# Performance work log

Measured on AMD Instinct MI355X. Metric: run time of the kernel, lower is better.

Reference implementation:

```python
import jax, jax.numpy as jnp
import numpy as np

B, N, C = 8, 2048, 512

def setup_inputs() -> dict:
    key = jax.random.key(0)
    k1, k2, k3 = jax.random.split(key, 3)
    x = jax.random.normal(k1, (B, N, C), dtype=jnp.float32)
    # xavier_uniform with gain=1.414 ~ uniform(-b, b), b = gain*sqrt(6/(fan_in+fan_out))
    bw = 1.414 * np.sqrt(6.0 / (C + C))
    w = jax.random.uniform(k2, (C, C), dtype=jnp.float32, minval=-bw, maxval=bw)
    ba = 1.414 * np.sqrt(6.0 / (2 * C + 1))
    a = jax.random.uniform(k3, (2 * C, 1), dtype=jnp.float32, minval=-ba, maxval=ba)
    return {"x": x, "w": w, "a": a}

def reference(x, w, a):
    # x: [B,N,C], w: [C,C], a: [2C,1]
    C_ = w.shape[0]
    h = jnp.matmul(x, w)                      # [B,N,C]
    a1 = a[:C_, 0]                            # [C]
    a2 = a[C_:, 0]                            # [C]
    # The torch repeat/cat/view builds e_ij = LeakyReLU(a1.h_i + a2.h_j);
    # compute the same math via broadcasting (no [B,N,N,2C] tensor).
    s1 = jnp.einsum('bnc,c->bn', h, a1)       # [B,N]
    s2 = jnp.einsum('bnc,c->bn', h, a2)       # [B,N]
    e = jax.nn.leaky_relu(s1[:, :, None] + s2[:, None, :], negative_slope=0.2)  # [B,N,N]
    attention = jax.nn.softmax(e, axis=2)     # softmax over source nodes j
    # dropout is identity in eval mode (training=False)
    h_prime = jnp.matmul(attention, x)        # [B,N,C]
    return h_prime
```

## Files before the change

kernel.cpp:

```cpp
#include <hip/hip_runtime.h>
#include <math.h>

#define B_ 8
#define N_ 2048
#define C_ 512
#define G_ 64
#define L_ 32

static const size_t OFF_V1   = 0;
static const size_t OFF_V2   = OFF_V1 + 512;
static const size_t OFF_S1   = OFF_V2 + 512;
static const size_t OFF_S2   = OFF_S1 + 16384;
static const size_t OFF_Z    = OFF_S2 + 16384;
static const size_t OFF_IDX  = OFF_Z + 16384;
static const size_t OFF_P    = OFF_IDX + 16384;
static const size_t OFF_Q    = OFF_P + 16384;
static const size_t OFF_CHP  = OFF_Q + 16384;
static const size_t OFF_CHQ  = OFF_CHP + 262144;
static const size_t OFF_TOTQ = OFF_CHQ + 262144;
static const size_t OFF_EMR  = OFF_TOTQ + 4096;
static const size_t OFF_EMP  = OFF_EMR + 16384;
static const size_t OFF_EMQ  = OFF_EMP + 16384;
static const size_t OFF_POS  = OFF_EMQ + 16384;

__device__ inline float4 f4z() { return make_float4(0.f, 0.f, 0.f, 0.f); }
__device__ inline float4 fma4(float s, float4 a, float4 c) {
    c.x = fmaf(s, a.x, c.x); c.y = fmaf(s, a.y, c.y);
    c.z = fmaf(s, a.z, c.z); c.w = fmaf(s, a.w, c.w); return c;
}
__device__ inline float4 add4(float4 a, float4 b) {
    return make_float4(a.x + b.x, a.y + b.y, a.z + b.z, a.w + b.w);
}
__device__ inline float4 comb4(float fp, float4 P, float fq, float4 T, float4 Q) {
    return make_float4(fp * P.x + fq * (T.x - Q.x),
                       fp * P.y + fq * (T.y - Q.y),
                       fp * P.z + fq * (T.z - Q.z),
                       fp * P.w + fq * (T.w - Q.w));
}

__global__ __launch_bounds__(64) void k_wa(const float* __restrict__ w,
                                           const float* __restrict__ a,
                                           float* __restrict__ v1, float* __restrict__ v2) {
    int k = blockIdx.x, lane = threadIdx.x;
    float acc1 = 0.f, acc2 = 0.f;
    for (int c = lane; c < C_; c += 64) {
        float wv = w[k * C_ + c];
        acc1 += wv * a[c];
        acc2 += wv * a[C_ + c];
    }
    for (int o = 32; o > 0; o >>= 1) { acc1 += __shfl_down(acc1, o); acc2 += __shfl_down(acc2, o); }
    if (lane == 0) { v1[k] = acc1; v2[k] = acc2; }
}

__global__ __launch_bounds__(256) void k_s(const float* __restrict__ x,
                                           const float* __restrict__ v1,
                                           const float* __restrict__ v2,
                                           float* __restrict__ s1, float* __restrict__ s2) {
    __shared__ __align__(16) float sv1[C_];
    __shared__ __align__(16) float sv2[C_];
    int tid = threadIdx.x;
    for (int c = tid; c < C_; c += 256) { sv1[c] = v1[c]; sv2[c] = v2[c]; }
    __syncthreads();
    int wave = tid >> 6, lane = tid & 63;
    int r = blockIdx.x * 4 + wave;
    const float4* xr  = reinterpret_cast<const float4*>(x + (size_t)r * C_);
    const float4* w1p = reinterpret_cast<const float4*>(sv1);
    const float4* w2p = reinterpret_cast<const float4*>(sv2);
    float a1 = 0.f, a2 = 0.f;
    #pragma unroll
    for (int half = 0; half < 2; ++half) {
        int c4 = lane + half * 64;
        float4 xv = xr[c4], w1 = w1p[c4], w2 = w2p[c4];
        a1 += xv.x*w1.x + xv.y*w1.y + xv.z*w1.z + xv.w*w1.w;
        a2 += xv.x*w2.x + xv.y*w2.y + xv.z*w2.z + xv.w*w2.w;
    }
    for (int o = 32; o > 0; o >>= 1) { a1 += __shfl_down(a1, o); a2 += __shfl_down(a2, o); }
    if (lane == 0) { s1[r] = a1; s2[r] = a2; }
}

__global__ __launch_bounds__(256) void k_rank(const float* __restrict__ s2,
                                              float* __restrict__ z, int* __restrict__ idxArr,
                                              float* __restrict__ pArr, float* __restrict__ qArr) {
    __shared__ float sval[N_];
    __shared__ float sred[256];
    __shared__ int   srnk[256];
    int blk = blockIdx.x;
    int b = blk >> 5, grp = blk & 31;
    int tid = threadIdx.x;
    int le = tid & 63, qtr = tid >> 6;
    for (int i = tid; i < N_; i += 256) sval[i] = s2[(size_t)b * N_ + i];
    __syncthreads();
    int e = grp * 64 + le;
    float val = sval[e];
    int base = qtr * 512;
    int rank = 0;
    float mx = -3.4e38f;
    #pragma unroll 8
    for (int i = 0; i < 512; ++i) {
        int t = base + i;
        float v = sval[t];
        mx = fmaxf(mx, v);
        rank += (v < val) || (v == val && t < e);
    }
    srnk[tid] = rank;
    sred[tid] = mx;
    __syncthreads();
    for (int o = 128; o > 0; o >>= 1) {
        if (tid < o) sred[tid] = fmaxf(sred[tid], sred[tid + o]);
        __syncthreads();
    }
    float m2 = sred[0];
    if (qtr == 0) {
        int rk = srnk[le] + srnk[le + 64] + srnk[le + 128] + srnk[le + 192];
        float d = val - m2;
        size_t pos = (size_t)b * N_ + rk;
        z[pos]      = val;
        idxArr[pos] = e;
        pArr[pos]   = __expf(d);
        qArr[pos]   = __expf(0.2f * d);
    }
}

__global__ __launch_bounds__(512) void k_chunk(const float* __restrict__ x,
                                               const int* __restrict__ idxArr,
                                               const float* __restrict__ pArr,
                                               const float* __restrict__ qArr,
                                               float* __restrict__ chP, float* __restrict__ chQ) {
    int bg = blockIdx.x, b = bg >> 6, g = bg & 63;
    int tid = threadIdx.x;
    __shared__ int   srow[L_];
    __shared__ float spv[L_], sqv[L_];
    __shared__ float4 partP[4][128], partQ[4][128];
    if (tid < L_) {
        int j = g * L_ + tid;
        srow[tid] = idxArr[b * N_ + j];
        spv[tid]  = pArr[b * N_ + j];
        sqv[tid]  = qArr[b * N_ + j];
    }
    __syncthreads();
    int rg = tid >> 7, q = tid & 127;
    const float4* xb4 = reinterpret_cast<const float4*>(x + (size_t)b * N_ * C_);
    float4 aP = f4z(), aQ = f4z();
    #pragma unroll
    for (int i = 0; i < 8; ++i) {
        int j = rg * 8 + i;
        float4 xv = xb4[(size_t)srow[j] * 128 + q];
        aP = fma4(spv[j], xv, aP);
        aQ = fma4(sqv[j], xv, aQ);
    }
    partP[rg][q] = aP;
    partQ[rg][q] = aQ;
    __syncthreads();
    if (tid < 128) {
        float4 s = add4(add4(partP[0][tid], partP[1][tid]), add4(partP[2][tid], partP[3][tid]));
        reinterpret_cast<float4*>(chP + (size_t)bg * C_)[tid] = s;
    } else if (tid < 256) {
        int qq = tid - 128;
        float4 s = add4(add4(partQ[0][qq], partQ[1][qq]), add4(partQ[2][qq], partQ[3][qq]));
        reinterpret_cast<float4*>(chQ + (size_t)bg * C_)[qq] = s;
    }
}

__global__ __launch_bounds__(128) void k_choff(float* __restrict__ chP, float* __restrict__ chQ,
                                               float* __restrict__ totQ) {
    int t = blockIdx.x * 128 + threadIdx.x;
    int isQ = t >> 12, rem = t & 4095;
    int b = rem >> 9, c = rem & 511;
    float* arr = isQ ? chQ : chP;
    float v[G_];
    #pragma unroll
    for (int g = 0; g < G_; ++g)
        v[g] = arr[((size_t)(b * G_ + g)) * C_ + c];
    float run = 0.f;
    #pragma unroll
    for (int g = G_ - 1; g >= 0; --g) {
        float tv = v[g];
        arr[((size_t)(b * G_ + g)) * C_ + c] = run;
        run += tv;
    }
    if (isQ) totQ[b * C_ + c] = run;
}

__global__ __launch_bounds__(1024) void k_prep(const float* __restrict__ s1,
                                               const float* __restrict__ z,
                                               const float* __restrict__ pArr,
                                               const float* __restrict__ qArr,
                                               int* __restrict__ emRow,
                                               float* __restrict__ emFP,
                                               float* __restrict__ emFQ,
                                               int* __restrict__ posStart) {
    __shared__ float Ppre[2049], Qpre[2049];
    __shared__ float zv[N_];
    __shared__ int   cnt[2049];
    __shared__ int   ps[2050];
    __shared__ float wsP[16], wsQ[16], woP[16], woQ[16];
    __shared__ int   wsC[16], woC[16];
    int b = blockIdx.x, tid = threadIdx.x, lane = tid & 63, wid = tid >> 6;
    size_t ib = (size_t)b * N_;

    for (int i = tid; i < 2049; i += 1024) cnt[i] = 0;
    zv[2*tid]   = z[ib + 2*tid];
    zv[2*tid+1] = z[ib + 2*tid+1];

    float p0 = pArr[ib + 2*tid], p1 = pArr[ib + 2*tid+1];
    float q0 = qArr[ib + 2*tid], q1 = qArr[ib + 2*tid+1];
    float pv = p0 + p1, qv = q0 + q1;
    float pi = pv, qi = qv;
    for (int o = 1; o < 64; o <<= 1) {
        float tp = __shfl_up(pi, o), tq2 = __shfl_up(qi, o);
        if (lane >= o) { pi += tp; qi += tq2; }
    }
    if (lane == 63) { wsP[wid] = pi; wsQ[wid] = qi; }
    __syncthreads();
    if (wid == 0 && lane < 16) {
        float sp = wsP[lane], sq = wsQ[lane];
        float ip = sp, iq = sq;
        for (int o = 1; o < 16; o <<= 1) {
            float tp = __shfl_up(ip, o), tq2 = __shfl_up(iq, o);
            if (lane >= o) { ip += tp; iq += tq2; }
        }
        woP[lane] = ip - sp; woQ[lane] = iq - sq;
    }
    __syncthreads();
    float inclP = pi + woP[wid], inclQ = qi + woQ[wid];
    float exclP = inclP - pv,    exclQ = inclQ - qv;
    Ppre[2*tid]   = exclP;  Ppre[2*tid+1] = exclP + p0;
    Qpre[2*tid]   = exclQ;  Qpre[2*tid+1] = exclQ + q0;
    if (tid == 1023) { Ppre[2048] = inclP; Qpre[2048] = inclQ; }
    __syncthreads();

    float m2   = zv[N_ - 1];
    float Ptot = Ppre[2048];
    int   kk[2], sl[2];
    float fPv[2], fQv[2];
    #pragma unroll
    for (int h = 0; h < 2; ++h) {
        int rl = tid + h * 1024;
        float s1v = s1[ib + rl];
        float thr = -s1v;
        int lo = 0, hi = N_;
        while (lo < hi) { int mid = (lo + hi) >> 1; if (zv[mid] >= thr) hi = mid; else lo = mid + 1; }
        float beta = s1v + m2;
        float wPc, wQc;
        if (beta >= 0.f) { wPc = 1.f;                  wQc = __expf(-0.8f * beta); }
        else             { wPc = __expf(0.8f * beta);  wQc = 1.f; }
        float Sp = Ptot - Ppre[lo];
        float Sq = Qpre[lo];
        float inv = 1.f / (wPc * Sp + wQc * Sq);
        fPv[h] = wPc * inv;
        fQv[h] = wQc * inv;
        kk[h] = lo;
        sl[h] = atomicAdd(&cnt[lo], 1);
    }
    __syncthreads();

    int c0 = cnt[2*tid], c1 = cnt[2*tid+1];
    int cv = c0 + c1, ci = cv;
    for (int o = 1; o < 64; o <<= 1) {
        int t2 = __shfl_up(ci, o);
        if (lane >= o) ci += t2;
    }
    if (lane == 63) wsC[wid] = ci;
    __syncthreads();
    if (wid == 0 && lane < 16) {
        int sc = wsC[lane], ic = sc;
        for (int o = 1; o < 16; o <<= 1) { int t2 = __shfl_up(ic, o); if (lane >= o) ic += t2; }
        woC[lane] = ic - sc;
    }
    __syncthreads();
    int inclC = ci + woC[wid];
    int exclC = inclC - cv;
    ps[2*tid] = exclC; ps[2*tid+1] = exclC + c0;
    if (tid == 1023) { ps[2048] = inclC; ps[2049] = inclC + cnt[2048]; }
    __syncthreads();
    posStart[b * 2050 + tid]        = ps[tid];
    posStart[b * 2050 + 1024 + tid] = ps[1024 + tid];
    if (tid < 2) posStart[b * 2050 + 2048 + tid] = ps[2048 + tid];
    #pragma unroll
    for (int h = 0; h < 2; ++h) {
        int rl = tid + h * 1024;
        int u  = ps[kk[h]] + sl[h];
        emRow[ib + u] = rl;
        emFP [ib + u] = fPv[h];
        emFQ [ib + u] = fQv[h];
    }
}

__global__ __launch_bounds__(512) void k_fused(const float* __restrict__ x,
                                               const int* __restrict__ idxArr,
                                               const float* __restrict__ pArr,
                                               const float* __restrict__ qArr,
                                               const float* __restrict__ chP,
                                               const float* __restrict__ chQ,
                                               const float* __restrict__ totQ,
                                               const int* __restrict__ emRow,
                                               const float* __restrict__ emFP,
                                               const float* __restrict__ emFQ,
                                               const int* __restrict__ posStart,
                                               float* __restrict__ out) {
    int bg = blockIdx.x, b = bg >> 6, g = bg & 63;
    int tid = threadIdx.x;
    __shared__ int   srow[L_];
    __shared__ float spv[L_], sqv[L_];
    __shared__ int   sps[L_ + 2];
    __shared__ int   semRow[N_];
    __shared__ float semFP[N_], semFQ[N_];
    __shared__ float4 partP[4][128], partQ[4][128];
    if (tid < L_) {
        int j = g * L_ + tid;
        srow[tid] = idxArr[b * N_ + j];
        spv[tid]  = pArr[b * N_ + j];
        sqv[tid]  = qArr[b * N_ + j];
    }
    if (tid >= 64 && tid < 64 + L_ + 2) sps[tid - 64] = posStart[b * 2050 + g * L_ + (tid - 64)];
    __syncthreads();
    int uStart = sps[0];
    int uEnd   = (g == G_ - 1) ? sps[L_ + 1] : sps[L_];
    size_t ib = (size_t)b * N_;
    for (int u = uStart + tid; u < uEnd; u += 512) {
        int e = u - uStart;
        semRow[e] = emRow[ib + u];
        semFP[e]  = emFP [ib + u];
        semFQ[e]  = emFQ [ib + u];
    }
    int rg = tid >> 7, q = tid & 127;
    const float4* xb4 = reinterpret_cast<const float4*>(x + (size_t)b * N_ * C_);
    float4 xr4[8];
    #pragma unroll
    for (int i = 0; i < 8; ++i)
        xr4[i] = xb4[(size_t)srow[rg * 8 + i] * 128 + q];
    float4 sP = f4z(), sQ = f4z();
    #pragma unroll
    for (int i = 0; i < 8; ++i) {
        int j = rg * 8 + i;
        sP = fma4(spv[j], xr4[i], sP);
        sQ = fma4(sqv[j], xr4[i], sQ);
    }
    partP[rg][q] = sP;
    partQ[rg][q] = sQ;
    __syncthreads();
    float4 runP = reinterpret_cast<const float4*>(chP + (size_t)bg * C_)[q];
    float4 runQ = reinterpret_cast<const float4*>(chQ + (size_t)bg * C_)[q];
    float4 tq4  = reinterpret_cast<const float4*>(totQ + (size_t)b * C_)[q];
    #pragma unroll
    for (int rg2 = 3; rg2 >= 1; --rg2) {
        if (rg2 > rg) { runP = add4(runP, partP[rg2][q]); runQ = add4(runQ, partQ[rg2][q]); }
    }
    float4* ob4 = reinterpret_cast<float4*>(out + (size_t)b * N_ * C_);
    if (g == G_ - 1 && rg == 3) {
        for (int u = sps[L_]; u < sps[L_ + 1]; ++u) {
            int e = u - uStart;
            ob4[(size_t)semRow[e] * 128 + q] = comb4(semFP[e], runP, semFQ[e], tq4, runQ);
        }
    }
    #pragma unroll
    for (int t = 7; t >= 0; --t) {
        int j = rg * 8 + t;
        runP = fma4(spv[j], xr4[t], runP);
        runQ = fma4(sqv[j], xr4[t], runQ);
        for (int u = sps[j]; u < sps[j + 1]; ++u) {
            int e = u - uStart;
            ob4[(size_t)semRow[e] * 128 + q] = comb4(semFP[e], runP, semFQ[e], tq4, runQ);
        }
    }
}

extern "C" void kernel_launch(void* const* d_in, const int* in_sizes, int n_in,
                              void* d_out, int out_size, void* d_ws, size_t ws_size,
                              hipStream_t stream) {
    const float* x = (const float*)d_in[0];
    const float* w = (const float*)d_in[1];
    const float* a = (const float*)d_in[2];
    float* out = (float*)d_out;
    float* ws  = (float*)d_ws;

    float* v1   = ws + OFF_V1;
    float* v2   = ws + OFF_V2;
    float* s1   = ws + OFF_S1;
    float* s2   = ws + OFF_S2;
    float* zArr = ws + OFF_Z;
    int*   idxA = (int*)(ws + OFF_IDX);
    float* pArr = ws + OFF_P;
    float* qArr = ws + OFF_Q;
    float* chP  = ws + OFF_CHP;
    float* chQ  = ws + OFF_CHQ;
    float* totQ = ws + OFF_TOTQ;
    int*   emR  = (int*)(ws + OFF_EMR);
    float* emP  = ws + OFF_EMP;
    float* emQ  = ws + OFF_EMQ;
    int*   pos  = (int*)(ws + OFF_POS);

    k_wa   <<<dim3(C_),      dim3(64),   0, stream>>>(w, a, v1, v2);
    k_s    <<<dim3(4096),    dim3(256),  0, stream>>>(x, v1, v2, s1, s2);
    k_rank <<<dim3(B_ * 32), dim3(256),  0, stream>>>(s2, zArr, idxA, pArr, qArr);
    k_chunk<<<dim3(B_ * G_), dim3(512),  0, stream>>>(x, idxA, pArr, qArr, chP, chQ);
    k_choff<<<dim3(64),      dim3(128),  0, stream>>>(chP, chQ, totQ);
    k_prep <<<dim3(B_),      dim3(1024), 0, stream>>>(s1, zArr, pArr, qArr, emR, emP, emQ, pos);
    k_fused<<<dim3(B_ * G_), dim3(512),  0, stream>>>(x, idxA, pArr, qArr, chP, chQ, totQ,
                                                      emR, emP, emQ, pos, out);
}
```

Baseline: 133.0 us.

## Merge chunk-sum and prep kernels, compute chunk offsets inside fused kernel

Combines the chunk partial-sum kernel and the per-batch prep kernel into one launch with a shared-memory union, so the small prep blocks run alongside the chunk blocks. It drops the separate chunk-offset scan kernel and the totQ buffer. Instead, each fused block sums the later chunk totals itself at startup. This removes two launches and a serial dependency, but every fused block now re-reads up to 64 chunk vectors, which adds redundant global reads.

```diff
diff --git a/kernel.cpp b/kernel.cpp
--- a/kernel.cpp
+++ b/kernel.cpp
@@ -17,8 +17,7 @@
 static const size_t OFF_Q    = OFF_P + 16384;
 static const size_t OFF_CHP  = OFF_Q + 16384;
 static const size_t OFF_CHQ  = OFF_CHP + 262144;
-static const size_t OFF_TOTQ = OFF_CHQ + 262144;
-static const size_t OFF_EMR  = OFF_TOTQ + 4096;
+static const size_t OFF_EMR  = OFF_CHQ + 262144;
 static const size_t OFF_EMP  = OFF_EMR + 16384;
 static const size_t OFF_EMQ  = OFF_EMP + 16384;
 static const size_t OFF_POS  = OFF_EMQ + 16384;
@@ -121,168 +120,135 @@
     }
 }
 
-__global__ __launch_bounds__(512) void k_chunk(const float* __restrict__ x,
-                                               const int* __restrict__ idxArr,
-                                               const float* __restrict__ pArr,
-                                               const float* __restrict__ qArr,
-                                               float* __restrict__ chP, float* __restrict__ chQ) {
-    int bg = blockIdx.x, b = bg >> 6, g = bg & 63;
-    int tid = threadIdx.x;
-    __shared__ int   srow[L_];
-    __shared__ float spv[L_], sqv[L_];
-    __shared__ float4 partP[4][128], partQ[4][128];
-    if (tid < L_) {
-        int j = g * L_ + tid;
-        srow[tid] = idxArr[b * N_ + j];
-        spv[tid]  = pArr[b * N_ + j];
-        sqv[tid]  = qArr[b * N_ + j];
-    }
-    __syncthreads();
-    int rg = tid >> 7, q = tid & 127;
-    const float4* xb4 = reinterpret_cast<const float4*>(x + (size_t)b * N_ * C_);
-    float4 aP = f4z(), aQ = f4z();
-    #pragma unroll
-    for (int i = 0; i < 8; ++i) {
-        int j = rg * 8 + i;
-        float4 xv = xb4[(size_t)srow[j] * 128 + q];
-        aP = fma4(spv[j], xv, aP);
-        aQ = fma4(sqv[j], xv, aQ);
-    }
-    partP[rg][q] = aP;
-    partQ[rg][q] = aQ;
-    __syncthreads();
-    if (tid < 128) {
-        float4 s = add4(add4(partP[0][tid], partP[1][tid]), add4(partP[2][tid], partP[3][tid]));
-        reinterpret_cast<float4*>(chP + (size_t)bg * C_)[tid] = s;
-    } else if (tid < 256) {
-        int qq = tid - 128;
-        float4 s = add4(add4(partQ[0][qq], partQ[1][qq]), add4(partQ[2][qq], partQ[3][qq]));
-        reinterpret_cast<float4*>(chQ + (size_t)bg * C_)[qq] = s;
-    }
-}
-
-__global__ __launch_bounds__(128) void k_choff(float* __restrict__ chP, float* __restrict__ chQ,
-                                               float* __restrict__ totQ) {
-    int t = blockIdx.x * 128 + threadIdx.x;
-    int isQ = t >> 12, rem = t & 4095;
-    int b = rem >> 9, c = rem & 511;
-    float* arr = isQ ? chQ : chP;
-    float v[G_];
-    #pragma unroll
-    for (int g = 0; g < G_; ++g)
-        v[g] = arr[((size_t)(b * G_ + g)) * C_ + c];
-    float run = 0.f;
-    #pragma unroll
-    for (int g = G_ - 1; g >= 0; --g) {
-        float tv = v[g];
-        arr[((size_t)(b * G_ + g)) * C_ + c] = run;
-        run += tv;
-    }
-    if (isQ) totQ[b * C_ + c] = run;
-}
-
-__global__ __launch_bounds__(1024) void k_prep(const float* __restrict__ s1,
-                                               const float* __restrict__ z,
-                                               const float* __restrict__ pArr,
-                                               const float* __restrict__ qArr,
-                                               int* __restrict__ emRow,
-                                               float* __restrict__ emFP,
-                                               float* __restrict__ emFQ,
-                                               int* __restrict__ posStart) {
-    __shared__ float Ppre[2049], Qpre[2049];
-    __shared__ float zv[N_];
-    __shared__ int   cnt[2049];
-    __shared__ int   ps[2050];
-    __shared__ float wsP[16], wsQ[16], woP[16], woQ[16];
-    __shared__ int   wsC[16], woC[16];
-    int b = blockIdx.x, tid = threadIdx.x, lane = tid & 63, wid = tid >> 6;
-    size_t ib = (size_t)b * N_;
-
-    for (int i = tid; i < 2049; i += 1024) cnt[i] = 0;
-    zv[2*tid]   = z[ib + 2*tid];
-    zv[2*tid+1] = z[ib + 2*tid+1];
-
-    float p0 = pArr[ib + 2*tid], p1 = pArr[ib + 2*tid+1];
-    float q0 = qArr[ib + 2*tid], q1 = qArr[ib + 2*tid+1];
-    float pv = p0 + p1, qv = q0 + q1;
-    float pi = pv, qi = qv;
-    for (int o = 1; o < 64; o <<= 1) {
-        float tp = __shfl_up(pi, o), tq2 = __shfl_up(qi, o);
-        if (lane >= o) { pi += tp; qi += tq2; }
-    }
-    if (lane == 63) { wsP[wid] = pi; wsQ[wid] = qi; }
-    __syncthreads();
-    if (wid == 0 && lane < 16) {
-        float sp = wsP[lane], sq = wsQ[lane];
-        float ip = sp, iq = sq;
-        for (int o = 1; o < 16; o <<= 1) {
-            float tp = __shfl_up(ip, o), tq2 = __shfl_up(iq, o);
-            if (lane >= o) { ip += tp; iq += tq2; }
-        }
-        woP[lane] = ip - sp; woQ[lane] = iq - sq;
-    }
-    __syncthreads();
-    float inclP = pi + woP[wid], inclQ = qi + woQ[wid];
-    float exclP = inclP - pv,    exclQ = inclQ - qv;
-    Ppre[2*tid]   = exclP;  Ppre[2*tid+1] = exclP + p0;
-    Qpre[2*tid]   = exclQ;  Qpre[2*tid+1] = exclQ + q0;
-    if (tid == 1023) { Ppre[2048] = inclP; Qpre[2048] = inclQ; }
-    __syncthreads();
-
-    float m2   = zv[N_ - 1];
-    float Ptot = Ppre[2048];
-    int   kk[2], sl[2];
-    float fPv[2], fQv[2];
-    #pragma unroll
-    for (int h = 0; h < 2; ++h) {
-        int rl = tid + h * 1024;
-        float s1v = s1[ib + rl];
-        float thr = -s1v;
-        int lo = 0, hi = N_;
-        while (lo < hi) { int mid = (lo + hi) >> 1; if (zv[mid] >= thr) hi = mid; else lo = mid + 1; }
-        float beta = s1v + m2;
-        float wPc, wQc;
-        if (beta >= 0.f) { wPc = 1.f;                  wQc = __expf(-0.8f * beta); }
-        else             { wPc = __expf(0.8f * beta);  wQc = 1.f; }
-        float Sp = Ptot - Ppre[lo];
-        float Sq = Qpre[lo];
-        float inv = 1.f / (wPc * Sp + wQc * Sq);
-        fPv[h] = wPc * inv;
-        fQv[h] = wQc * inv;
-        kk[h] = lo;
-        sl[h] = atomicAdd(&cnt[lo], 1);
-    }
-    __syncthreads();
-
-    int c0 = cnt[2*tid], c1 = cnt[2*tid+1];
-    int cv = c0 + c1, ci = cv;
-    for (int o = 1; o < 64; o <<= 1) {
-        int t2 = __shfl_up(ci, o);
-        if (lane >= o) ci += t2;
-    }
-    if (lane == 63) wsC[wid] = ci;
-    __syncthreads();
-    if (wid == 0 && lane < 16) {
-        int sc = wsC[lane], ic = sc;
-        for (int o = 1; o < 16; o <<= 1) { int t2 = __shfl_up(ic, o); if (lane >= o) ic += t2; }
-        woC[lane] = ic - sc;
-    }
-    __syncthreads();
-    int inclC = ci + woC[wid];
-    int exclC = inclC - cv;
-    ps[2*tid] = exclC; ps[2*tid+1] = exclC + c0;
-    if (tid == 1023) { ps[2048] = inclC; ps[2049] = inclC + cnt[2048]; }
-    __syncthreads();
-    posStart[b * 2050 + tid]        = ps[tid];
-    posStart[b * 2050 + 1024 + tid] = ps[1024 + tid];
-    if (tid < 2) posStart[b * 2050 + 2048 + tid] = ps[2048 + tid];
-    #pragma unroll
-    for (int h = 0; h < 2; ++h) {
-        int rl = tid + h * 1024;
-        int u  = ps[kk[h]] + sl[h];
-        emRow[ib + u] = rl;
-        emFP [ib + u] = fPv[h];
-        emFQ [ib + u] = fQv[h];
+__global__ __launch_bounds__(1024) void k_cp(const float* __restrict__ x,
+                                             const int* __restrict__ idxArr,
+                                             const float* __restrict__ pArr,
+                                             const float* __restrict__ qArr,
+                                             const float* __restrict__ s1,
+                                             const float* __restrict__ z,
+                                             float* __restrict__ chP, float* __restrict__ chQ,
+                                             int* __restrict__ emRow,
+                                             float* __restrict__ emFP,
+                                             float* __restrict__ emFQ,
+                                             int* __restrict__ posStart) {
+    union CpSM {
+        struct {
+            int srow[2][L_]; float spv[2][L_], sqv[2][L_];
+            float4 partP[2][4][128], partQ[2][4][128];
+        } ch;
+        struct {
+            float Ppre[N_ + 1], Qpre[N_ + 1], zv[N_];
+            int cnt[N_ + 1], ps[N_ + 2];
+            float wsP[16], wsQ[16], woP[16], woQ[16];
+            int wsC[16], woC[16];
+        } pr;
+    };
+    __shared__ CpSM sm;
+    int gid = blockIdx.x, tid = threadIdx.x;
+    int lane = tid & 63, wid = tid >> 6;
+
+    if (gid < 256) {
+        int h = tid >> 9, t2 = tid & 511;
+        int job = gid * 2 + h, b = job >> 6, g = job & 63;
+        if (t2 < L_) {
+            size_t jb = (size_t)b * N_ + g * L_ + t2;
+            sm.ch.srow[h][t2] = idxArr[jb];
+            sm.ch.spv[h][t2]  = pArr[jb];
+            sm.ch.sqv[h][t2]  = qArr[jb];
+        }
+        __syncthreads();
+        int rg = t2 >> 7, q = t2 & 127;
+        const float4* xb4 = reinterpret_cast<const float4*>(x + (size_t)b * N_ * C_);
+        float4 aP = f4z(), aQ = f4z();
+        #pragma unroll
+        for (int i = 0; i < 8; ++i) {
+            int j = rg * 8 + i;
+            float4 xv = xb4[(size_t)sm.ch.srow[h][j] * 128 + q];
+            aP = fma4(sm.ch.spv[h][j], xv, aP);
+            aQ = fma4(sm.ch.sqv[h][j], xv, aQ);
+        }
+        sm.ch.partP[h][rg][q] = aP;
+        sm.ch.partQ[h][rg][q] = aQ;
+        __syncthreads();
+        if (t2 < 128) {
+            float4 s = add4(add4(sm.ch.partP[h][0][t2], sm.ch.partP[h][1][t2]),
+                            add4(sm.ch.partP[h][2][t2], sm.ch.partP[h][3][t2]));
+            reinterpret_cast<float4*>(chP + (size_t)job * C_)[t2] = s;
+        } else if (t2 < 256) {
+            int qq = t2 - 128;
+            float4 s = add4(add4(sm.ch.partQ[h][0][qq], sm.ch.partQ[h][1][qq]),
+                            add4(sm.ch.partQ[h][2][qq], sm.ch.partQ[h][3][qq]));
+            reinterpret_cast<float4*>(chQ + (size_t)job * C_)[qq] = s;
+        }
+    } else {
+        int b = gid - 256;
+        size_t ib = (size_t)b * N_;
+        for (int i = tid; i < N_ + 1; i += 1024) sm.pr.cnt[i] = 0;
+        sm.pr.zv[2*tid]   = z[ib + 2*tid];
+        sm.pr.zv[2*tid+1] = z[ib + 2*tid+1];
+        float p0 = pArr[ib + 2*tid], p1 = pArr[ib + 2*tid+1];
+        float q0 = qArr[ib + 2*tid], q1 = qArr[ib + 2*tid+1];
+        float pv = p0 + p1, qv = q0 + q1, pi = pv, qi = qv;
+        for (int o = 1; o < 64; o <<= 1) {
+            float tp = __shfl_up(pi, o), tq2 = __shfl_up(qi, o);
+            if (lane >= o) { pi += tp; qi += tq2; }
+        }
+        if (lane == 63) { sm.pr.wsP[wid] = pi; sm.pr.wsQ[wid] = qi; }
+        __syncthreads();
+        if (wid == 0 && lane < 16) {
+            float sp = sm.pr.wsP[lane], sq = sm.pr.wsQ[lane], ip = sp, iq = sq;
+            for (int o = 1; o < 16; o <<= 1) {
+                float tp = __shfl_up(ip, o), tq2 = __shfl_up(iq, o);
+                if (lane >= o) { ip += tp; iq += tq2; }
+            }
+            sm.pr.woP[lane] = ip - sp; sm.pr.woQ[lane] = iq - sq;
+        }
+        __syncthreads();
+        float inclP = pi + sm.pr.woP[wid], inclQ = qi + sm.pr.woQ[wid];
+        float exclP = inclP - pv, exclQ = inclQ - qv;
+        sm.pr.Ppre[2*tid] = exclP; sm.pr.Ppre[2*tid+1] = exclP + p0;
+        sm.pr.Qpre[2*tid] = exclQ; sm.pr.Qpre[2*tid+1] = exclQ + q0;
+        if (tid == 1023) { sm.pr.Ppre[N_] = inclP; sm.pr.Qpre[N_] = inclQ; }
+        __syncthreads();
+        float m2 = sm.pr.zv[N_ - 1], Ptot = sm.pr.Ppre[N_];
+        int kk[2], sl[2]; float fPv[2], fQv[2];
+        #pragma unroll
+        for (int h = 0; h < 2; ++h) {
+            int rl = tid + h * 1024;
+            float s1v = s1[ib + rl], thr = -s1v;
+            int lo = 0, hi = N_;
+            while (lo < hi) { int mid = (lo + hi) >> 1; if (sm.pr.zv[mid] >= thr) hi = mid; else lo = mid + 1; }
+            float beta = s1v + m2, wPc, wQc;
+            if (beta >= 0.f) { wPc = 1.f;                 wQc = __expf(-0.8f * beta); }
+            else             { wPc = __expf(0.8f * beta); wQc = 1.f; }
+            float inv = 1.f / (wPc * (Ptot - sm.pr.Ppre[lo]) + wQc * sm.pr.Qpre[lo]);
+            fPv[h] = wPc * inv; fQv[h] = wQc * inv; kk[h] = lo;
+            sl[h] = atomicAdd(&sm.pr.cnt[lo], 1);
+        }
+        __syncthreads();
+        int c0 = sm.pr.cnt[2*tid], c1 = sm.pr.cnt[2*tid+1], cv = c0 + c1, ci = cv;
+        for (int o = 1; o < 64; o <<= 1) { int t2 = __shfl_up(ci, o); if (lane >= o) ci += t2; }
+        if (lane == 63) sm.pr.wsC[wid] = ci;
+        __syncthreads();
+        if (wid == 0 && lane < 16) {
+            int sc = sm.pr.wsC[lane], ic = sc;
+            for (int o = 1; o < 16; o <<= 1) { int t2 = __shfl_up(ic, o); if (lane >= o) ic += t2; }
+            sm.pr.woC[lane] = ic - sc;
+        }
+        __syncthreads();
+        int inclC = ci + sm.pr.woC[wid], exclC = inclC - cv;
+        sm.pr.ps[2*tid] = exclC; sm.pr.ps[2*tid+1] = exclC + c0;
+        if (tid == 1023) { sm.pr.ps[N_] = inclC; sm.pr.ps[N_+1] = inclC + sm.pr.cnt[N_]; }
+        __syncthreads();
+        posStart[b * 2050 + tid]        = sm.pr.ps[tid];
+        posStart[b * 2050 + 1024 + tid] = sm.pr.ps[1024 + tid];
+        if (tid < 2) posStart[b * 2050 + 2048 + tid] = sm.pr.ps[2048 + tid];
+        #pragma unroll
+        for (int h = 0; h < 2; ++h) {
+            int rl = tid + h * 1024;
+            int u = sm.pr.ps[kk[h]] + sl[h];
+            emRow[ib + u] = rl; emFP[ib + u] = fPv[h]; emFQ[ib + u] = fQv[h];
+        }
     }
 }
 
@@ -292,7 +258,6 @@
                                                const float* __restrict__ qArr,
                                                const float* __restrict__ chP,
                                                const float* __restrict__ chQ,
-                                               const float* __restrict__ totQ,
                                                const int* __restrict__ emRow,
                                                const float* __restrict__ emFP,
                                                const float* __restrict__ emFQ,
@@ -306,13 +271,30 @@
     __shared__ int   semRow[N_];
     __shared__ float semFP[N_], semFQ[N_];
     __shared__ float4 partP[4][128], partQ[4][128];
+    __shared__ float4 sOffP[128], sOffQ[128], sTq[128];
     if (tid < L_) {
         int j = g * L_ + tid;
         srow[tid] = idxArr[b * N_ + j];
         spv[tid]  = pArr[b * N_ + j];
         sqv[tid]  = qArr[b * N_ + j];
-    }
-    if (tid >= 64 && tid < 64 + L_ + 2) sps[tid - 64] = posStart[b * 2050 + g * L_ + (tid - 64)];
+    } else if (tid >= 32 && tid < 32 + L_ + 2) {
+        sps[tid - 32] = posStart[b * 2050 + g * L_ + (tid - 32)];
+    } else if (tid >= 128 && tid < 256) {
+        int q = tid - 128;
+        const float4* cp4 = reinterpret_cast<const float4*>(chP) + (size_t)b * G_ * 128;
+        float4 oP = f4z();
+        for (int g2 = G_ - 1; g2 > g; --g2) oP = add4(oP, cp4[g2 * 128 + q]);
+        sOffP[q] = oP;
+    } else if (tid >= 256 && tid < 384) {
+        int q = tid - 256;
+        const float4* cq4 = reinterpret_cast<const float4*>(chQ) + (size_t)b * G_ * 128;
+        float4 oQ = f4z();
+        for (int g2 = G_ - 1; g2 > g; --g2) oQ = add4(oQ, cq4[g2 * 128 + q]);
+        sOffQ[q] = oQ;
+        float4 tq = oQ;
+        for (int g2 = g; g2 >= 0; --g2) tq = add4(tq, cq4[g2 * 128 + q]);
+        sTq[q] = tq;
+    }
     __syncthreads();
     int uStart = sps[0];
     int uEnd   = (g == G_ - 1) ? sps[L_ + 1] : sps[L_];
@@ -339,9 +321,9 @@
     partP[rg][q] = sP;
     partQ[rg][q] = sQ;
     __syncthreads();
-    float4 runP = reinterpret_cast<const float4*>(chP + (size_t)bg * C_)[q];
-    float4 runQ = reinterpret_cast<const float4*>(chQ + (size_t)bg * C_)[q];
-    float4 tq4  = reinterpret_cast<const float4*>(totQ + (size_t)b * C_)[q];
+    float4 runP = sOffP[q];
+    float4 runQ = sOffQ[q];
+    float4 tq4  = sTq[q];
     #pragma unroll
     for (int rg2 = 3; rg2 >= 1; --rg2) {
         if (rg2 > rg) { runP = add4(runP, partP[rg2][q]); runQ = add4(runQ, partQ[rg2][q]); }
@@ -384,7 +366,6 @@
     float* qArr = ws + OFF_Q;
     float* chP  = ws + OFF_CHP;
     float* chQ  = ws + OFF_CHQ;
-    float* totQ = ws + OFF_TOTQ;
     int*   emR  = (int*)(ws + OFF_EMR);
     float* emP  = ws + OFF_EMP;
     float* emQ  = ws + OFF_EMQ;
@@ -393,9 +374,8 @@
     k_wa   <<<dim3(C_),      dim3(64),   0, stream>>>(w, a, v1, v2);
     k_s    <<<dim3(4096),    dim3(256),  0, stream>>>(x, v1, v2, s1, s2);
     k_rank <<<dim3(B_ * 32), dim3(256),  0, stream>>>(s2, zArr, idxA, pArr, qArr);
-    k_chunk<<<dim3(B_ * G_), dim3(512),  0, stream>>>(x, idxA, pArr, qArr, chP, chQ);
-    k_choff<<<dim3(64),      dim3(128),  0, stream>>>(chP, chQ, totQ);
-    k_prep <<<dim3(B_),      dim3(1024), 0, stream>>>(s1, zArr, pArr, qArr, emR, emP, emQ, pos);
-    k_fused<<<dim3(B_ * G_), dim3(512),  0, stream>>>(x, idxA, pArr, qArr, chP, chQ, totQ,
+    k_cp   <<<dim3(264),     dim3(1024), 0, stream>>>(x, idxA, pArr, qArr, s1, zArr,
+                                                      chP, chQ, emR, emP, emQ, pos);
+    k_fused<<<dim3(B_ * G_), dim3(512),  0, stream>>>(x, idxA, pArr, qArr, chP, chQ,
                                                       emR, emP, emQ, pos, out);
 }
```

Result: slower. 143.6 us (+8.0%).
